# Kernel tuning notes

Hardware: AMD Instinct MI355X
Metric: run time of the kernel (lower is better)

The kernel has to match this reference:

```python
import jax, jax.numpy as jnp
import numpy as np

EPS = 1e-5


def adder_conv(x, w, stride, padding):
    """AdderNet conv: out[n,o,i,j] = -sum_k |patch[n,i,j,k] - w[o,k]|.
    x: [N, Cin, H, W], w: [Cout, Cin, kh, kw]."""
    Cout, Cin, kh, kw = w.shape
    # patches: [N, Cin*kh*kw, Ho, Wo]
    p = jax.lax.conv_general_dilated_patches(
        x, (kh, kw), (stride, stride), [(padding, padding), (padding, padding)])
    p = jnp.transpose(p, (0, 2, 3, 1))  # [N, Ho, Wo, K]
    wf = w.reshape(Cout, Cin * kh * kw)  # [Cout, K]
    # sequential map over output channels bounds peak memory to one [N,Ho,Wo,K]
    # abs-diff tensor at a time (no huge [N,Cout,Ho,Wo,K] broadcast)
    def one_out(wo):
        return jnp.sum(jnp.abs(p - wo), axis=-1)  # [N, Ho, Wo]
    out = jax.lax.map(one_out, wf)  # [Cout, N, Ho, Wo]
    return -jnp.transpose(out, (1, 0, 2, 3))  # [N, Cout, Ho, Wo]


def bn_relu6(x, gamma, beta):
    # training-mode BatchNorm2d (batch statistics, biased variance) + ReLU6
    mean = jnp.mean(x, axis=(0, 2, 3), keepdims=True)
    var = jnp.var(x, axis=(0, 2, 3), keepdims=True)
    y = (x - mean) * jax.lax.rsqrt(var + EPS)
    y = y * gamma.reshape(1, -1, 1, 1) + beta.reshape(1, -1, 1, 1)
    return jnp.clip(y, 0.0, 6.0)


def setup_inputs() -> dict:
    key = jax.random.key(0)
    ks = jax.random.split(key, 20)
    f32 = jnp.float32

    def wgt(k, shape):
        return jax.random.normal(k, shape, f32) * 0.05

    def bn(k, c):
        k1, k2 = jax.random.split(k)
        g = 1.0 + 0.1 * jax.random.normal(k1, (c,), f32)
        b = 0.1 * jax.random.normal(k2, (c,), f32)
        return g, b

    x = jax.random.normal(ks[0], (16, 512, 38, 38), f32)
    w1 = wgt(ks[1], (256, 512, 1, 1)); g1, b1 = bn(ks[7], 256)
    w2 = wgt(ks[2], (512, 256, 3, 3)); g2, b2 = bn(ks[8], 512)
    w3 = wgt(ks[3], (128, 512, 1, 1)); g3, b3 = bn(ks[9], 128)
    w4 = wgt(ks[4], (256, 128, 3, 3)); g4, b4 = bn(ks[10], 256)
    w5 = wgt(ks[5], (128, 256, 1, 1)); g5, b5 = bn(ks[11], 128)
    w6 = wgt(ks[6], (256, 128, 3, 3)); g6, b6 = bn(ks[12], 256)
    return {"x": x,
            "w1": w1, "g1": g1, "b1": b1,
            "w2": w2, "g2": g2, "b2": b2,
            "w3": w3, "g3": g3, "b3": b3,
            "w4": w4, "g4": g4, "b4": b4,
            "w5": w5, "g5": g5, "b5": b5,
            "w6": w6, "g6": g6, "b6": b6}


def reference(x, w1, g1, b1, w2, g2, b2, w3, g3, b3,
              w4, g4, b4, w5, g5, b5, w6, g6, b6):
    x = bn_relu6(adder_conv(x, w1, 1, 0), g1, b1)  # [N,256,38,38]
    x = bn_relu6(adder_conv(x, w2, 2, 1), g2, b2)  # [N,512,19,19]
    x = bn_relu6(adder_conv(x, w3, 1, 0), g3, b3)  # [N,128,19,19]
    x = bn_relu6(adder_conv(x, w4, 2, 1), g4, b4)  # [N,256,10,10]
    x = bn_relu6(adder_conv(x, w5, 1, 0), g5, b5)  # [N,128,10,10]
    x = bn_relu6(adder_conv(x, w6, 2, 0), g6, b6)  # [N,256,4,4]
    return x
```

## Files before the change

### kernel.cpp

```cpp
#include <hip/hip_runtime.h>


#define QSCALE 131072.0f
#define QBIAS  1048576.5f
#define QINV   7.62939453125e-06

template <bool IS3x3, bool BN>
__global__ __launch_bounds__(256, 4)
void adder_conv(const float* __restrict__ x, const unsigned* __restrict__ wT,
                const float2* __restrict__ ab, unsigned* __restrict__ part,
                int Cin, int H, int W, int Wo, int Cout,
                int stride, int pad, int cpz, int P, int PI, int Pp)
{
    constexpr int KC = 32;
    __shared__ unsigned xs[KC][68];
    __shared__ unsigned ws[KC][128];
    __shared__ float2 abls[512];

    const int t  = threadIdx.x;
    const int tx = t & 15, ty = t >> 4;
    const int ptile = blockIdx.x * 64, otile = blockIdx.y * 128;
    const int pp = t & 63, rg = t >> 6;
    const int oq = t & 31, kr = t >> 5;

    if (BN) {
        for (int i = t; i < Cin; i += 256) abls[i] = ab[i];
        __syncthreads();
    }

    const int p_st = ptile + pp;
    const bool pv = p_st < P;
    int n_st = 0, q = 0;
    if (pv) { n_st = p_st / PI; q = p_st - n_st * PI; }
    const int oh = q / Wo, ow = q - oh * Wo;
    const int ih0 = oh * stride - pad, iw0 = ow * stride - pad;
    const int HWi = H * W;
    const float* xb = x + (size_t)n_st * Cin * HWi;
    const unsigned* wbase = wT + otile + oq * 4;

    unsigned acc[4][8] = {};

    const int chunkBeg = blockIdx.z * cpz, chunkEnd = chunkBeg + cpz;

    float xr0, xr1, xr2, xr3, xr4, xr5, xr6, xr7;
    uint4 wr0, wr1, wr2, wr3;
    int c0P = 0; bool vP = false;

#define ISSUE(CH) do {                                                        \
        const int k0_ = (CH) * KC;                                            \
        int c0_, ih_, iw_;                                                    \
        if (IS3x3) {                                                          \
            const int tap_ = k0_ / Cin;               \
            c0_ = k0_ - tap_ * Cin;                                           \
            const int kh_ = tap_ / 3, kw_ = tap_ - kh_ * 3;                   \
            ih_ = ih0 + kh_; iw_ = iw0 + kw_;                                 \
        } else { c0_ = k0_; ih_ = ih0; iw_ = iw0; }                           \
        vP = pv && (!IS3x3 || (ih_ >= 0 && ih_ < H && iw_ >= 0 && iw_ < W));  \
        c0P = c0_;                                                            \
        const float* px_ = xb + (size_t)(c0_ + rg) * HWi + (ih_ * W + iw_);   \
        xr0 = vP ? px_[0] : 0.f;                                              \
        xr1 = vP ? px_[(size_t) 4 * HWi] : 0.f;                               \
        xr2 = vP ? px_[(size_t) 8 * HWi] : 0.f;                               \
        xr3 = vP ? px_[(size_t)12 * HWi] : 0.f;                               \
        xr4 = vP ? px_[(size_t)16 * HWi] : 0.f;                               \
        xr5 = vP ? px_[(size_t)20 * HWi] : 0.f;                               \
        xr6 = vP ? px_[(size_t)24 * HWi] : 0.f;                               \
        xr7 = vP ? px_[(size_t)28 * HWi] : 0.f;                               \
        const unsigned* pw_ = wbase + (size_t)(k0_ + kr) * Cout;              \
        wr0 = *(const uint4*)(pw_);                                           \
        wr1 = *(const uint4*)(pw_ + (size_t) 8 * Cout);                       \
        wr2 = *(const uint4*)(pw_ + (size_t)16 * Cout);                       \
        wr3 = *(const uint4*)(pw_ + (size_t)24 * Cout);                       \
    } while (0)

#define BNQ(V, J, DST)                                                        \
        {                                                                     \
            float vv_ = V;                                                    \
            if (BN) {                                                         \
                const float2 s_ = abls[c0P + rg + 4 * (J)];                   \
                vv_ = fminf(fmaxf(fmaf(s_.x, vv_, s_.y), 0.f), 6.f);          \
                vv_ = vP ? vv_ : 0.f;            \
            }                                                                 \
            DST = (unsigned)fmaf(vv_, QSCALE, QBIAS);                         \
        }

#define WRITE_LDS() do {                                                      \
        unsigned q0_, q1_, q2_, q3_, q4_, q5_, q6_, q7_;                      \
        BNQ(xr0, 0, q0_) BNQ(xr1, 1, q1_) BNQ(xr2, 2, q2_) BNQ(xr3, 3, q3_)   \
        BNQ(xr4, 4, q4_) BNQ(xr5, 5, q5_) BNQ(xr6, 6, q6_) BNQ(xr7, 7, q7_)   \
        xs[rg     ][pp] = q0_; xs[rg +  4][pp] = q1_;                         \
        xs[rg +  8][pp] = q2_; xs[rg + 12][pp] = q3_;                         \
        xs[rg + 16][pp] = q4_; xs[rg + 20][pp] = q5_;                         \
        xs[rg + 24][pp] = q6_; xs[rg + 28][pp] = q7_;                         \
        *(uint4*)&ws[kr     ][oq * 4] = wr0;                                  \
        *(uint4*)&ws[kr +  8][oq * 4] = wr1;                                  \
        *(uint4*)&ws[kr + 16][oq * 4] = wr2;                                  \
        *(uint4*)&ws[kr + 24][oq * 4] = wr3;                                  \
    } while (0)

    ISSUE(chunkBeg);

    for (int ch = chunkBeg; ch < chunkEnd; ++ch) {
        WRITE_LDS();
        if (ch + 1 < chunkEnd) ISSUE(ch + 1);
        asm volatile("s_waitcnt lgkmcnt(0)" ::: "memory");
        __builtin_amdgcn_s_barrier();
        asm volatile("" ::: "memory");

#pragma unroll 2
        for (int kk = 0; kk < KC; ++kk) {
            const uint4 xv = *(const uint4*)&xs[kk][tx * 4];
            const uint4 wa = *(const uint4*)&ws[kk][ty * 8];
            const uint4 wb = *(const uint4*)&ws[kk][ty * 8 + 4];
#define S1(A, XC, WC) asm("v_sad_u32 %0, %1, %2, %0" : "+v"(A) : "v"(XC), "v"(WC));
#define SROW(I, XC)                                             \
            S1(acc[I][0], XC, wa.x) S1(acc[I][1], XC, wa.y)     \
            S1(acc[I][2], XC, wa.z) S1(acc[I][3], XC, wa.w)     \
            S1(acc[I][4], XC, wb.x) S1(acc[I][5], XC, wb.y)     \
            S1(acc[I][6], XC, wb.z) S1(acc[I][7], XC, wb.w)
            SROW(0, xv.x) SROW(1, xv.y) SROW(2, xv.z) SROW(3, xv.w)
#undef SROW
#undef S1
        }
        asm volatile("" ::: "memory");
        __builtin_amdgcn_s_barrier();
        asm volatile("" ::: "memory");
    }
#undef ISSUE
#undef BNQ
#undef WRITE_LDS

    const int p0 = ptile + tx * 4;
    const bool full = (p0 + 3) < P;
#pragma unroll
    for (int jj = 0; jj < 8; ++jj) {
        const int o = otile + ty * 8 + jj;
        unsigned* dst = part + ((size_t)blockIdx.z * Cout + o) * Pp + p0;
        if (full) {
            *(uint4*)dst = make_uint4(acc[0][jj], acc[1][jj], acc[2][jj], acc[3][jj]);
        } else {
#pragma unroll
            for (int i = 0; i < 4; ++i)
                if (p0 + i < P) dst[i] = acc[i][jj];
        }
    }
}

__global__ void combine_stats(const unsigned* __restrict__ part, float* __restrict__ fin,
                              double* __restrict__ st, int C, int PI, int Z, int Pp)
{
    const int c = blockIdx.x, n = blockIdx.y, t = threadIdx.x;
    const int pbase = n * PI;
    double s = 0.0, s2 = 0.0;
    for (int qq = t; qq < PI; qq += 256) {
        unsigned long long u = 0;
        for (int z = 0; z < Z; ++z)
            u += part[((size_t)z * C + c) * Pp + pbase + qq];
        const float v = -(float)((double)u * QINV);
        fin[((size_t)n * C + c) * PI + qq] = v;
        s += v; s2 += (double)v * v;
    }
    __shared__ double sh[256], sh2[256];
    sh[t] = s; sh2[t] = s2; __syncthreads();
    for (int off = 128; off > 0; off >>= 1) {
        if (t < off) { sh[t] += sh[t + off]; sh2[t] += sh2[t + off]; }
        __syncthreads();
    }
    if (t == 0) {
        unsafeAtomicAdd(&st[2 * c], sh[0]);
        unsafeAtomicAdd(&st[2 * c + 1], sh2[0]);
    }
}

__global__ void ab_kernel(const double* __restrict__ st, const float* __restrict__ gamma,
                          const float* __restrict__ beta, float2* __restrict__ ab,
                          int C, double invCount)
{
    const int c = blockIdx.x * blockDim.x + threadIdx.x;
    if (c < C) {
        const double mean = st[2 * c] * invCount;
        const double var  = st[2 * c + 1] * invCount - mean * mean;
        const float a = gamma[c] * rsqrtf((float)var + 1e-5f);
        const float b = beta[c] - (float)mean * a;
        ab[c] = make_float2(a, b);
    }
}

__global__ void apply_kernel(const float* __restrict__ y, const float2* __restrict__ ab,
                             float* __restrict__ out, int total, int C, int PI)
{
    const int i = blockIdx.x * 256 + threadIdx.x;
    if (i < total) {
        const int c = (i / PI) % C;
        const float2 s = ab[c];
        out[i] = fminf(fmaxf(fmaf(s.x, y[i], s.y), 0.f), 6.f);
    }
}

struct TDesc { const float* w; unsigned* wT; int Cout; int Cin; int Tap; int elems; };
struct TPack { TDesc d[6]; };

__global__ void transpose_all(TPack p)
{
    const TDesc d = p.d[blockIdx.y];
    const int i = blockIdx.x * 256 + threadIdx.x;
    if (i < d.elems) {
        const int k = i / d.Cout, o = i - k * d.Cout;
        const int tap = k / d.Cin, c = k - tap * d.Cin;
        const float v = d.w[((size_t)o * d.Cin + c) * d.Tap + tap];
        d.wT[i] = (unsigned)fmaf(v, QSCALE, QBIAS);
    }
}

extern "C" void kernel_launch(void* const* d_in, const int* in_sizes, int n_in,
                              void* d_out, int out_size, void* d_ws, size_t ws_size,
                              hipStream_t stream)
{
    const float* x = (const float*)d_in[0];
    const float *w[6], *g[6], *bt[6];
    for (int i = 0; i < 6; ++i) {
        w[i]  = (const float*)d_in[1 + 3 * i];
        g[i]  = (const float*)d_in[2 + 3 * i];
        bt[i] = (const float*)d_in[3 + 3 * i];
    }

    const size_t partSmall = 23658496, partBig = 47316992;
    const size_t wTbytes = 7995392;
    const size_t fixedBytes = 23658496 + 11829248 + wTbytes + 3072 * 8 + 1536 * 8;
    const bool big = ws_size >= fixedBytes + partBig;
    const size_t partBytes = big ? partBig : partSmall;

    char* ws = (char*)d_ws;
    float* bufA = (float*)ws;
    float* bufB = (float*)(ws + 23658496);
    unsigned* part = (unsigned*)(ws + 23658496 + 11829248);
    size_t off = 23658496 + 11829248 + partBytes;
    const int wElems[6] = {256 * 512, 512 * 2304, 128 * 512,
                           256 * 1152, 128 * 256, 256 * 1152};
    unsigned* wT[6];
    for (int i = 0; i < 6; ++i) { wT[i] = (unsigned*)(ws + off); off += (size_t)wElems[i] * 4; }
    double* st = (double*)(ws + off); off += 3072 * 8;
    float2* ab = (float2*)(ws + off);
    const int stOff[6] = {0, 512, 1536, 1792, 2304, 2560};
    const int abOff[6] = {0, 256, 768, 896, 1152, 1280};

    const int zL1 = big ? 2 : 1,  cpzL1 = 16 / zL1;
    const int zL2 = big ? 4 : 2,  cpzL2 = 72 / zL2;
    const int zL3 = big ? 16 : 8, cpzL3 = 16 / zL3;
    const int zL4 = big ? 18 : 12, cpzL4 = 36 / zL4;
    const int zL5 = 8,            cpzL5 = 1;
    const int zL6 = big ? 36 : 18, cpzL6 = 36 / zL6;

    const dim3 blk(256);

    hipMemsetAsync(st, 0, 3072 * 8, stream);

    TPack tp;
    const int wCout[6] = {256, 512, 128, 256, 128, 256};
    const int wCin[6]  = {512, 256, 512, 128, 256, 128};
    const int wTap[6]  = {1, 9, 1, 9, 1, 9};
    for (int i = 0; i < 6; ++i)
        tp.d[i] = TDesc{w[i], wT[i], wCout[i], wCin[i], wTap[i], wElems[i]};
    transpose_all<<<dim3((1179648 + 255) / 256, 6), blk, 0, stream>>>(tp);

    adder_conv<false, false><<<dim3(361, 2, zL1), blk, 0, stream>>>(
        x, wT[0], nullptr, part, 512, 38, 38, 38, 256, 1, 0, cpzL1, 23104, 1444, 23104);
    combine_stats<<<dim3(256, 16), blk, 0, stream>>>(part, bufA, st + stOff[0], 256, 1444, zL1, 23104);
    ab_kernel<<<1, blk, 0, stream>>>(st + stOff[0], g[0], bt[0], ab + abOff[0], 256, 1.0 / 23104);

    adder_conv<true, true><<<dim3(91, 4, zL2), blk, 0, stream>>>(
        bufA, wT[1], ab + abOff[0], part, 256, 38, 38, 19, 512, 2, 1, cpzL2, 5776, 361, 5776);
    combine_stats<<<dim3(512, 16), blk, 0, stream>>>(part, bufB, st + stOff[1], 512, 361, zL2, 5776);
    ab_kernel<<<2, blk, 0, stream>>>(st + stOff[1], g[1], bt[1], ab + abOff[1], 512, 1.0 / 5776);

    adder_conv<false, true><<<dim3(91, 1, zL3), blk, 0, stream>>>(
        bufB, wT[2], ab + abOff[1], part, 512, 19, 19, 19, 128, 1, 0, cpzL3, 5776, 361, 5776);
    combine_stats<<<dim3(128, 16), blk, 0, stream>>>(part, bufA, st + stOff[2], 128, 361, zL3, 5776);
    ab_kernel<<<1, blk, 0, stream>>>(st + stOff[2], g[2], bt[2], ab + abOff[2], 128, 1.0 / 5776);

    adder_conv<true, true><<<dim3(25, 2, zL4), blk, 0, stream>>>(
        bufA, wT[3], ab + abOff[2], part, 128, 19, 19, 10, 256, 2, 1, cpzL4, 1600, 100, 1600);
    combine_stats<<<dim3(256, 16), blk, 0, stream>>>(part, bufB, st + stOff[3], 256, 100, zL4, 1600);
    ab_kernel<<<1, blk, 0, stream>>>(st + stOff[3], g[3], bt[3], ab + abOff[3], 256, 1.0 / 1600);

    adder_conv<false, true><<<dim3(25, 1, zL5), blk, 0, stream>>>(
        bufB, wT[4], ab + abOff[3], part, 256, 10, 10, 10, 128, 1, 0, cpzL5, 1600, 100, 1600);
    combine_stats<<<dim3(128, 16), blk, 0, stream>>>(part, bufA, st + stOff[4], 128, 100, zL5, 1600);
    ab_kernel<<<1, blk, 0, stream>>>(st + stOff[4], g[4], bt[4], ab + abOff[4], 128, 1.0 / 1600);

    adder_conv<true, true><<<dim3(4, 2, zL6), blk, 0, stream>>>(
        bufA, wT[5], ab + abOff[4], part, 128, 10, 10, 4, 256, 2, 0, cpzL6, 256, 16, 256);
    combine_stats<<<dim3(256, 16), blk, 0, stream>>>(part, bufB, st + stOff[5], 256, 16, zL6, 256);
    ab_kernel<<<1, blk, 0, stream>>>(st + stOff[5], g[5], bt[5], ab + abOff[5], 256, 1.0 / 256);

    apply_kernel<<<(65536 + 255) / 256, blk, 0, stream>>>(bufB, ab + abOff[5], (float*)d_out,
                                                          65536, 256, 16);
}
```

Before: 656.4 us.

## Add 256-wide output-channel tile variant for adder conv layers 1 and 2

```diff
diff --git a/kernel.cpp b/kernel.cpp
--- a/kernel.cpp
+++ b/kernel.cpp
@@ -5,8 +5,8 @@
 #define QBIAS  1048576.5f
 #define QINV   7.62939453125e-06
 
-template <bool IS3x3, bool BN>
-__global__ __launch_bounds__(256, 4)
+template <bool IS3x3, bool BN, int OCH>
+__global__ __launch_bounds__(256, OCH == 256 ? 3 : 4)
 void adder_conv(const float* __restrict__ x, const unsigned* __restrict__ wT,
                 const float2* __restrict__ ab, unsigned* __restrict__ part,
                 int Cin, int H, int W, int Wo, int Cout,
@@ -14,14 +14,17 @@
 {
     constexpr int KC = 32;
     __shared__ unsigned xs[KC][68];
-    __shared__ unsigned ws[KC][128];
+    __shared__ unsigned ws[KC][OCH];
     __shared__ float2 abls[512];
 
     const int t  = threadIdx.x;
-    const int tx = t & 15, ty = t >> 4;
-    const int ptile = blockIdx.x * 64, otile = blockIdx.y * 128;
+    const int px = (OCH == 256) ? (t & 7) : (t & 15);
+    const int oc = (OCH == 256) ? (t >> 3) : (t >> 4);
+    const int ptile = blockIdx.x * 64, otile = blockIdx.y * OCH;
     const int pp = t & 63, rg = t >> 6;
-    const int oq = t & 31, kr = t >> 5;
+    const int woq = (OCH == 256) ? (t & 63) : (t & 31);
+    const int wkr = (OCH == 256) ? (t >> 6) : (t >> 5);
+    constexpr int WSTEP = (OCH == 256) ? 4 : 8;
 
     if (BN) {
         for (int i = t; i < Cin; i += 256) abls[i] = ab[i];
@@ -36,14 +39,15 @@
     const int ih0 = oh * stride - pad, iw0 = ow * stride - pad;
     const int HWi = H * W;
     const float* xb = x + (size_t)n_st * Cin * HWi;
-    const unsigned* wbase = wT + otile + oq * 4;
+    const unsigned* wbase = wT + otile + woq * 4;
 
     unsigned acc[4][8] = {};
+    unsigned acc2[2][4][8] = {};
 
     const int chunkBeg = blockIdx.z * cpz, chunkEnd = chunkBeg + cpz;
 
     float xr0, xr1, xr2, xr3, xr4, xr5, xr6, xr7;
-    uint4 wr0, wr1, wr2, wr3;
+    uint4 wr0, wr1, wr2, wr3, wr4, wr5, wr6, wr7;
     int c0P = 0; bool vP = false;
 
 #define ISSUE(CH) do {                                                        \
@@ -66,11 +70,17 @@
         xr5 = vP ? px_[(size_t)20 * HWi] : 0.f;                               \
         xr6 = vP ? px_[(size_t)24 * HWi] : 0.f;                               \
         xr7 = vP ? px_[(size_t)28 * HWi] : 0.f;                               \
-        const unsigned* pw_ = wbase + (size_t)(k0_ + kr) * Cout;              \
+        const unsigned* pw_ = wbase + (size_t)(k0_ + wkr) * Cout;             \
         wr0 = *(const uint4*)(pw_);                                           \
-        wr1 = *(const uint4*)(pw_ + (size_t) 8 * Cout);                       \
-        wr2 = *(const uint4*)(pw_ + (size_t)16 * Cout);                       \
-        wr3 = *(const uint4*)(pw_ + (size_t)24 * Cout);                       \
+        wr1 = *(const uint4*)(pw_ + (size_t)(1 * WSTEP) * Cout);              \
+        wr2 = *(const uint4*)(pw_ + (size_t)(2 * WSTEP) * Cout);              \
+        wr3 = *(const uint4*)(pw_ + (size_t)(3 * WSTEP) * Cout);              \
+        if (OCH == 256) {                                                     \
+            wr4 = *(const uint4*)(pw_ + (size_t)(4 * WSTEP) * Cout);          \
+            wr5 = *(const uint4*)(pw_ + (size_t)(5 * WSTEP) * Cout);          \
+            wr6 = *(const uint4*)(pw_ + (size_t)(6 * WSTEP) * Cout);          \
+            wr7 = *(const uint4*)(pw_ + (size_t)(7 * WSTEP) * Cout);          \
+        }                                                                     \
     } while (0)
 
 #define BNQ(V, J, DST)                                                        \
@@ -92,10 +102,16 @@
         xs[rg +  8][pp] = q2_; xs[rg + 12][pp] = q3_;                         \
         xs[rg + 16][pp] = q4_; xs[rg + 20][pp] = q5_;                         \
         xs[rg + 24][pp] = q6_; xs[rg + 28][pp] = q7_;                         \
-        *(uint4*)&ws[kr     ][oq * 4] = wr0;                                  \
-        *(uint4*)&ws[kr +  8][oq * 4] = wr1;                                  \
-        *(uint4*)&ws[kr + 16][oq * 4] = wr2;                                  \
-        *(uint4*)&ws[kr + 24][oq * 4] = wr3;                                  \
+        *(uint4*)&ws[wkr            ][woq * 4] = wr0;                         \
+        *(uint4*)&ws[wkr + 1 * WSTEP][woq * 4] = wr1;                         \
+        *(uint4*)&ws[wkr + 2 * WSTEP][woq * 4] = wr2;                         \
+        *(uint4*)&ws[wkr + 3 * WSTEP][woq * 4] = wr3;                         \
+        if (OCH == 256) {                                                     \
+            *(uint4*)&ws[wkr + 4 * WSTEP][woq * 4] = wr4;                     \
+            *(uint4*)&ws[wkr + 5 * WSTEP][woq * 4] = wr5;                     \
+            *(uint4*)&ws[wkr + 6 * WSTEP][woq * 4] = wr6;                     \
+            *(uint4*)&ws[wkr + 7 * WSTEP][woq * 4] = wr7;                     \
+        }                                                                     \
     } while (0)
 
     ISSUE(chunkBeg);
@@ -107,21 +123,39 @@
         __builtin_amdgcn_s_barrier();
         asm volatile("" ::: "memory");
 
+#define S1(A, XC, WC) asm("v_sad_u32 %0, %1, %2, %0" : "+v"(A) : "v"(XC), "v"(WC));
+        if (OCH == 128) {
 #pragma unroll 2
-        for (int kk = 0; kk < KC; ++kk) {
-            const uint4 xv = *(const uint4*)&xs[kk][tx * 4];
-            const uint4 wa = *(const uint4*)&ws[kk][ty * 8];
-            const uint4 wb = *(const uint4*)&ws[kk][ty * 8 + 4];
-#define S1(A, XC, WC) asm("v_sad_u32 %0, %1, %2, %0" : "+v"(A) : "v"(XC), "v"(WC));
+            for (int kk = 0; kk < KC; ++kk) {
+                const uint4 xv = *(const uint4*)&xs[kk][px * 4];
+                const uint4 wa = *(const uint4*)&ws[kk][oc * 8];
+                const uint4 wb = *(const uint4*)&ws[kk][oc * 8 + 4];
 #define SROW(I, XC)                                             \
-            S1(acc[I][0], XC, wa.x) S1(acc[I][1], XC, wa.y)     \
-            S1(acc[I][2], XC, wa.z) S1(acc[I][3], XC, wa.w)     \
-            S1(acc[I][4], XC, wb.x) S1(acc[I][5], XC, wb.y)     \
-            S1(acc[I][6], XC, wb.z) S1(acc[I][7], XC, wb.w)
-            SROW(0, xv.x) SROW(1, xv.y) SROW(2, xv.z) SROW(3, xv.w)
+                S1(acc[I][0], XC, wa.x) S1(acc[I][1], XC, wa.y) \
+                S1(acc[I][2], XC, wa.z) S1(acc[I][3], XC, wa.w) \
+                S1(acc[I][4], XC, wb.x) S1(acc[I][5], XC, wb.y) \
+                S1(acc[I][6], XC, wb.z) S1(acc[I][7], XC, wb.w)
+                SROW(0, xv.x) SROW(1, xv.y) SROW(2, xv.z) SROW(3, xv.w)
 #undef SROW
+            }
+        } else {
+#pragma unroll 2
+            for (int kk = 0; kk < KC; ++kk) {
+                const uint4 xlo = *(const uint4*)&xs[kk][px * 4];
+                const uint4 xhi = *(const uint4*)&xs[kk][32 + px * 4];
+                const uint4 wlo = *(const uint4*)&ws[kk][oc * 4];
+                const uint4 whi = *(const uint4*)&ws[kk][128 + oc * 4];
+#define SROW(a, i, XC)                                                \
+                S1(acc2[a][i][0], XC, wlo.x) S1(acc2[a][i][1], XC, wlo.y) \
+                S1(acc2[a][i][2], XC, wlo.z) S1(acc2[a][i][3], XC, wlo.w) \
+                S1(acc2[a][i][4], XC, whi.x) S1(acc2[a][i][5], XC, whi.y) \
+                S1(acc2[a][i][6], XC, whi.z) S1(acc2[a][i][7], XC, whi.w)
+                SROW(0, 0, xlo.x) SROW(0, 1, xlo.y) SROW(0, 2, xlo.z) SROW(0, 3, xlo.w)
+                SROW(1, 0, xhi.x) SROW(1, 1, xhi.y) SROW(1, 2, xhi.z) SROW(1, 3, xhi.w)
+#undef SROW
+            }
+        }
 #undef S1
-        }
         asm volatile("" ::: "memory");
         __builtin_amdgcn_s_barrier();
         asm volatile("" ::: "memory");
@@ -130,18 +164,39 @@
 #undef BNQ
 #undef WRITE_LDS
 
-    const int p0 = ptile + tx * 4;
-    const bool full = (p0 + 3) < P;
-#pragma unroll
-    for (int jj = 0; jj < 8; ++jj) {
-        const int o = otile + ty * 8 + jj;
-        unsigned* dst = part + ((size_t)blockIdx.z * Cout + o) * Pp + p0;
-        if (full) {
-            *(uint4*)dst = make_uint4(acc[0][jj], acc[1][jj], acc[2][jj], acc[3][jj]);
-        } else {
-#pragma unroll
-            for (int i = 0; i < 4; ++i)
-                if (p0 + i < P) dst[i] = acc[i][jj];
+    if (OCH == 128) {
+        const int p0 = ptile + px * 4;
+        const bool full = (p0 + 3) < P;
+#pragma unroll
+        for (int jj = 0; jj < 8; ++jj) {
+            const int o = otile + oc * 8 + jj;
+            unsigned* dst = part + ((size_t)blockIdx.z * Cout + o) * Pp + p0;
+            if (full) {
+                *(uint4*)dst = make_uint4(acc[0][jj], acc[1][jj], acc[2][jj], acc[3][jj]);
+            } else {
+#pragma unroll
+                for (int i = 0; i < 4; ++i)
+                    if (p0 + i < P) dst[i] = acc[i][jj];
+            }
+        }
+    } else {
+#pragma unroll
+        for (int a = 0; a < 2; ++a) {
+            const int p0 = ptile + a * 32 + px * 4;
+            const bool full = (p0 + 3) < P;
+#pragma unroll
+            for (int jj = 0; jj < 8; ++jj) {
+                const int o = otile + (jj < 4 ? oc * 4 + jj : 128 + oc * 4 + (jj - 4));
+                unsigned* dst = part + ((size_t)blockIdx.z * Cout + o) * Pp + p0;
+                if (full) {
+                    *(uint4*)dst = make_uint4(acc2[a][0][jj], acc2[a][1][jj],
+                                              acc2[a][2][jj], acc2[a][3][jj]);
+                } else {
+#pragma unroll
+                    for (int i = 0; i < 4; ++i)
+                        if (p0 + i < P) dst[i] = acc2[a][i][jj];
+                }
+            }
         }
     }
 }
@@ -244,11 +299,11 @@
     const int stOff[6] = {0, 512, 1536, 1792, 2304, 2560};
     const int abOff[6] = {0, 256, 768, 896, 1152, 1280};
 
-    const int zL1 = big ? 2 : 1,  cpzL1 = 16 / zL1;
-    const int zL2 = big ? 4 : 2,  cpzL2 = 72 / zL2;
-    const int zL3 = big ? 16 : 8, cpzL3 = 16 / zL3;
+    const int zL1 = big ? 2 : 1,   cpzL1 = 16 / zL1;
+    const int zL2 = big ? 4 : 2,   cpzL2 = 72 / zL2;
+    const int zL3 = big ? 16 : 8,  cpzL3 = 16 / zL3;
     const int zL4 = big ? 18 : 12, cpzL4 = 36 / zL4;
-    const int zL5 = 8,            cpzL5 = 1;
+    const int zL5 = 8,             cpzL5 = 1;
     const int zL6 = big ? 36 : 18, cpzL6 = 36 / zL6;
 
     const dim3 blk(256);
@@ -263,32 +318,32 @@
         tp.d[i] = TDesc{w[i], wT[i], wCout[i], wCin[i], wTap[i], wElems[i]};
     transpose_all<<<dim3((1179648 + 255) / 256, 6), blk, 0, stream>>>(tp);
 
-    adder_conv<false, false><<<dim3(361, 2, zL1), blk, 0, stream>>>(
+    adder_conv<false, false, 256><<<dim3(361, 1, zL1), blk, 0, stream>>>(
         x, wT[0], nullptr, part, 512, 38, 38, 38, 256, 1, 0, cpzL1, 23104, 1444, 23104);
     combine_stats<<<dim3(256, 16), blk, 0, stream>>>(part, bufA, st + stOff[0], 256, 1444, zL1, 23104);
     ab_kernel<<<1, blk, 0, stream>>>(st + stOff[0], g[0], bt[0], ab + abOff[0], 256, 1.0 / 23104);
 
-    adder_conv<true, true><<<dim3(91, 4, zL2), blk, 0, stream>>>(
+    adder_conv<true, true, 256><<<dim3(91, 2, zL2), blk, 0, stream>>>(
         bufA, wT[1], ab + abOff[0], part, 256, 38, 38, 19, 512, 2, 1, cpzL2, 5776, 361, 5776);
     combine_stats<<<dim3(512, 16), blk, 0, stream>>>(part, bufB, st + stOff[1], 512, 361, zL2, 5776);
     ab_kernel<<<2, blk, 0, stream>>>(st + stOff[1], g[1], bt[1], ab + abOff[1], 512, 1.0 / 5776);
 
-    adder_conv<false, true><<<dim3(91, 1, zL3), blk, 0, stream>>>(
+    adder_conv<false, true, 128><<<dim3(91, 1, zL3), blk, 0, stream>>>(
         bufB, wT[2], ab + abOff[1], part, 512, 19, 19, 19, 128, 1, 0, cpzL3, 5776, 361, 5776);
     combine_stats<<<dim3(128, 16), blk, 0, stream>>>(part, bufA, st + stOff[2], 128, 361, zL3, 5776);
     ab_kernel<<<1, blk, 0, stream>>>(st + stOff[2], g[2], bt[2], ab + abOff[2], 128, 1.0 / 5776);
 
-    adder_conv<true, true><<<dim3(25, 2, zL4), blk, 0, stream>>>(
+    adder_conv<true, true, 128><<<dim3(25, 2, zL4), blk, 0, stream>>>(
         bufA, wT[3], ab + abOff[2], part, 128, 19, 19, 10, 256, 2, 1, cpzL4, 1600, 100, 1600);
     combine_stats<<<dim3(256, 16), blk, 0, stream>>>(part, bufB, st + stOff[3], 256, 100, zL4, 1600);
     ab_kernel<<<1, blk, 0, stream>>>(st + stOff[3], g[3], bt[3], ab + abOff[3], 256, 1.0 / 1600);
 
-    adder_conv<false, true><<<dim3(25, 1, zL5), blk, 0, stream>>>(
+    adder_conv<false, true, 128><<<dim3(25, 1, zL5), blk, 0, stream>>>(
         bufB, wT[4], ab + abOff[3], part, 256, 10, 10, 10, 128, 1, 0, cpzL5, 1600, 100, 1600);
     combine_stats<<<dim3(128, 16), blk, 0, stream>>>(part, bufA, st + stOff[4], 128, 100, zL5, 1600);
     ab_kernel<<<1, blk, 0, stream>>>(st + stOff[4], g[4], bt[4], ab + abOff[4], 128, 1.0 / 1600);
 
-    adder_conv<true, true><<<dim3(4, 2, zL6), blk, 0, stream>>>(
+    adder_conv<true, true, 128><<<dim3(4, 2, zL6), blk, 0, stream>>>(
         bufA, wT[5], ab + abOff[4], part, 128, 10, 10, 4, 256, 2, 0, cpzL6, 256, 16, 256);
     combine_stats<<<dim3(256, 16), blk, 0, stream>>>(part, bufB, st + stOff[5], 256, 16, zL6, 256);
     ab_kernel<<<1, blk, 0, stream>>>(st + stOff[5], g[5], bt[5], ab + abOff[5], 256, 1.0 / 256);
```

Measured after the change: 647.1 us. No clear change (-1.4%).
